# Performance work log

Hardware: AMD Instinct MI355X
Metric: run time of the kernel (lower is better)

The kernel has to match this reference:

```python
import jax, jax.numpy as jnp
import numpy as np
from jax import lax

B, T, N, C = 32, 32, 64, 64          # batch, window, num_series, inter_dim
GRU_H, QK, HOR = 64, 32, 12          # gru_dim, qk_dim, prediction_horizon
KS = (3, 5, 7)                       # temporal kernel per block (3 + 2*i)


def setup_inputs() -> dict:
    key = jax.random.key(0)
    ks = jax.random.split(key, 32)
    rn = lambda k, shape, s=0.05: jax.random.normal(k, shape, jnp.float32) * s
    inp = {"x": jax.random.normal(ks[0], (B, T, N), jnp.float32)}
    # x_to_inter_dim: Conv1d(1, C, kernel_size=1) == scalar * w + b
    inp["w_x2i"] = rn(ks[1], (C,)); inp["b_x2i"] = rn(ks[2], (C,))
    # latentCorrelation GRU (input_size=1, hidden=GRU_H), gate order r,z,n
    inp["gru_wih"] = rn(ks[3], (3 * GRU_H, 1)); inp["gru_whh"] = rn(ks[4], (3 * GRU_H, GRU_H))
    inp["gru_bih"] = rn(ks[5], (3 * GRU_H,)); inp["gru_bhh"] = rn(ks[6], (3 * GRU_H,))
    inp["wq_w"] = rn(ks[7], (QK, GRU_H)); inp["wq_b"] = rn(ks[8], (QK,))
    inp["wk_w"] = rn(ks[9], (QK, GRU_H)); inp["wk_b"] = rn(ks[10], (QK,))
    # per block: T independent GCNConvs (theta + bias), one temporal Conv1d
    for i, k_ in enumerate(KS):
        inp[f"gcn_w{i}"] = rn(ks[11 + 4 * i], (T, C, C))
        inp[f"gcn_b{i}"] = rn(ks[12 + 4 * i], (T, C))
        inp[f"conv_w{i}"] = rn(ks[13 + 4 * i], (C, C, k_))
        inp[f"conv_b{i}"] = rn(ks[14 + 4 * i], (C,))
    inp["lout_w"] = rn(ks[25], (N * HOR, T * N * C), 0.01)
    inp["lout_b"] = rn(ks[26], (N * HOR,))
    return inp


def _forward(x, w_x2i, b_x2i, gru_wih, gru_whh, gru_bih, gru_bhh,
             wq_w, wq_b, wk_w, wk_b,
             gcn_w0, gcn_b0, conv_w0, conv_b0,
             gcn_w1, gcn_b1, conv_w1, conv_b1,
             gcn_w2, gcn_b2, conv_w2, conv_b2,
             lout_w, lout_b):
    xs = jnp.transpose(x, (1, 0, 2))  # (T, B, N) time-major

    # --- latentCorrelation: one GRU run over all B*N series at once ---
    def gru_step(h, xt):  # h: (B,N,GRU_H), xt: (B,N)
        gi = xt[..., None] * gru_wih[:, 0] + gru_bih           # (B,N,3H)
        gh = h @ gru_whh.T + gru_bhh                           # (B,N,3H)
        r = jax.nn.sigmoid(gi[..., :GRU_H] + gh[..., :GRU_H])
        z = jax.nn.sigmoid(gi[..., GRU_H:2 * GRU_H] + gh[..., GRU_H:2 * GRU_H])
        n = jnp.tanh(gi[..., 2 * GRU_H:] + r * gh[..., 2 * GRU_H:])
        return (1.0 - z) * n + z * h, None

    h0 = jnp.zeros((B, N, GRU_H), x.dtype)
    hT, _ = lax.scan(gru_step, h0, xs)                         # (B,N,GRU_H)
    Q = hT @ wq_w.T + wq_b                                     # (B,N,QK)
    K = hT @ wk_w.T + wk_b
    Wadj = jax.nn.softmax(jnp.einsum('bnq,bmq->bnm', Q, K) / jnp.sqrt(jnp.float32(QK)), axis=2)

    # GCN symmetric norm on the dense complete graph; edge (src=i, tgt=j) has
    # weight Wadj[b,i,j]; degree is per-target (column) sum.
    deg = Wadj.sum(axis=1)                                     # (B,N)
    dinv = jnp.where(deg > 0, 1.0 / jnp.sqrt(deg), 0.0)
    What = dinv[:, :, None] * Wadj * dinv[:, None, :]          # (B,N,N)

    # x_to_inter_dim (1x1 conv) applied per timestep
    feats = xs[..., None] * w_x2i + b_x2i                      # (T,B,N,C)

    for gw, gb, cw, cb, k_ in ((gcn_w0, gcn_b0, conv_w0, conv_b0, 3),
                               (gcn_w1, gcn_b1, conv_w1, conv_b1, 5),
                               (gcn_w2, gcn_b2, conv_w2, conv_b2, 7)):
        xw = jnp.einsum('tbnc,tcd->tbnd', feats, gw)           # per-timestep theta
        agg = jnp.einsum('bij,tbid->tbjd', What, xw) + gb[:, None, None, :]
        seq = jnp.transpose(agg, (1, 2, 3, 0)).reshape(B * N, C, T)
        p = k_ // 2
        conv = lax.conv_general_dilated(seq, cw, (1,), [(p, p)],
                                        dimension_numbers=('NCH', 'OIH', 'NCH'))
        conv = conv + cb[None, :, None]
        conv = jnp.where(conv >= 0, conv, 0.01 * conv)         # LeakyReLU (dropout p=0)
        feats = jnp.transpose(conv.reshape(B, N, C, T), (3, 0, 1, 2))

    # stack(x_list, dim=2).view(B*N, C*T).view(B, -1) -> (B, N*C*T) feature order (n,c,t)
    flat = jnp.transpose(feats, (1, 2, 3, 0)).reshape(B, N * C * T)
    out = flat @ lout_w.T + lout_b                             # (B, N*HOR)
    return out.reshape(B, HOR, N)


def reference(x, w_x2i, b_x2i, gru_wih, gru_whh, gru_bih, gru_bhh,
              wq_w, wq_b, wk_w, wk_b,
              gcn_w0, gcn_b0, conv_w0, conv_b0,
              gcn_w1, gcn_b1, conv_w1, conv_b1,
              gcn_w2, gcn_b2, conv_w2, conv_b2,
              lout_w, lout_b):
    return _forward(x, w_x2i, b_x2i, gru_wih, gru_whh, gru_bih, gru_bhh,
                    wq_w, wq_b, wk_w, wk_b,
                    gcn_w0, gcn_b0, conv_w0, conv_b0,
                    gcn_w1, gcn_b1, conv_w1, conv_b1,
                    gcn_w2, gcn_b2, conv_w2, conv_b2,
                    lout_w, lout_b)
```

## Files before the change

### kernel.cpp

```cpp
#include <hip/hip_runtime.h>
#include <hip/hip_bf16.h>

#define BB 32
#define TT 32
#define NN 64
#define CC 64
#define HH 64
#define QKD 32
#define HOR 12
#define OUTD (NN*HOR)
#define KFLAT (NN*CC*TT)

typedef __attribute__((ext_vector_type(4))) float f32x4;
typedef __attribute__((ext_vector_type(8))) short s16x8;

static __device__ __forceinline__ unsigned short f2bf(float f) {
    unsigned u = __float_as_uint(f);
    unsigned r = (u + 0x7FFFu + ((u >> 16) & 1u)) >> 16;
    return (unsigned short)r;
}
static __device__ __forceinline__ float bf2f(unsigned short h) {
    return __uint_as_float(((unsigned)h) << 16);
}
static __device__ __forceinline__ void split8(const float* f, uint4& hi, uint4& lo) {
    unsigned hh[8], ll[8];
    #pragma unroll
    for (int i = 0; i < 8; ++i) {
        unsigned short h = f2bf(f[i]);
        float hf = bf2f(h);
        hh[i] = h;
        ll[i] = f2bf(f[i] - hf);
    }
    hi = make_uint4(hh[0] | (hh[1] << 16), hh[2] | (hh[3] << 16),
                    hh[4] | (hh[5] << 16), hh[6] | (hh[7] << 16));
    lo = make_uint4(ll[0] | (ll[1] << 16), ll[2] | (ll[3] << 16),
                    ll[4] | (ll[5] << 16), ll[6] | (ll[7] << 16));
}

__global__ __launch_bounds__(256) void gru_kernel(
    const float* __restrict__ x, const float* __restrict__ wih,
    const float* __restrict__ whh, const float* __restrict__ bih,
    const float* __restrict__ bhh, float* __restrict__ hT)
{
    __shared__ float Wt[64][192];
    __shared__ float hbuf[4][64];
    __shared__ float part[4][4][3][64];
    int tid = threadIdx.x;
    for (int idx = tid; idx < 192*64; idx += 256) {
        int g = idx >> 6, k = idx & 63;
        Wt[k][g] = whh[idx];
    }
    int w = tid >> 6;
    int j = tid & 63;
    hbuf[w][j] = 0.0f;
    __syncthreads();
    float Wreg[3][16];
    #pragma unroll
    for (int g = 0; g < 3; ++g)
        #pragma unroll
        for (int kk = 0; kk < 16; ++kk)
            Wreg[g][kk] = Wt[w*16 + kk][g*64 + j];
    int gs0 = blockIdx.x * 4;
    int b = gs0 >> 6, n0 = gs0 & 63;
    float wih_r = wih[j], wih_z = wih[64+j], wih_n = wih[128+j];
    float bi_r = bih[j], bi_z = bih[64+j], bi_n = bih[128+j];
    float bh_r = bhh[j], bh_z = bhh[64+j], bh_n = bhh[128+j];
    float hreg = 0.0f;
    for (int t = 0; t < TT; ++t) {
        float p[3][4];
        #pragma unroll
        for (int g = 0; g < 3; ++g)
            #pragma unroll
            for (int s = 0; s < 4; ++s) p[g][s] = 0.f;
        #pragma unroll
        for (int s = 0; s < 4; ++s) {
            #pragma unroll
            for (int q = 0; q < 4; ++q) {
                const float4 hv = *(const float4*)&hbuf[s][w*16 + q*4];
                #pragma unroll
                for (int g = 0; g < 3; ++g) {
                    p[g][s] += hv.x*Wreg[g][q*4]   + hv.y*Wreg[g][q*4+1]
                             + hv.z*Wreg[g][q*4+2] + hv.w*Wreg[g][q*4+3];
                }
            }
        }
        #pragma unroll
        for (int g = 0; g < 3; ++g)
            #pragma unroll
            for (int s = 0; s < 4; ++s)
                part[w][s][g][j] = p[g][s];
        __syncthreads();
        float gr = bh_r + part[0][w][0][j] + part[1][w][0][j] + part[2][w][0][j] + part[3][w][0][j];
        float gz = bh_z + part[0][w][1][j] + part[1][w][1][j] + part[2][w][1][j] + part[3][w][1][j];
        float gn = bh_n + part[0][w][2][j] + part[1][w][2][j] + part[2][w][2][j] + part[3][w][2][j];
        float xt = x[(b*TT + t)*NN + n0 + w];
        float r = 1.f/(1.f+__expf(-(xt*wih_r + bi_r + gr)));
        float z = 1.f/(1.f+__expf(-(xt*wih_z + bi_z + gz)));
        float nn_ = tanhf(xt*wih_n + bi_n + r*gn);
        float hnew = (1.f - z)*nn_ + z*hreg;
        hreg = hnew;
        hbuf[w][j] = hnew;
        __syncthreads();
    }
    hT[(gs0 + w)*64 + j] = hreg;
}

__global__ __launch_bounds__(256) void attn_kernel(
    const float* __restrict__ hT, const float* __restrict__ wq_w,
    const float* __restrict__ wq_b, const float* __restrict__ wk_w,
    const float* __restrict__ wk_b,
    unsigned short* __restrict__ whT_hi, unsigned short* __restrict__ whT_lo)
{
    __shared__ float hs[64][64];
    __shared__ float Qs[64][32], Ks[64][32];
    __shared__ float S[64][64];
    __shared__ float dinv[64];
    int b = blockIdx.x, tid = threadIdx.x;
    for (int idx = tid; idx < 64*64; idx += 256) hs[idx>>6][idx&63] = hT[b*4096 + idx];
    __syncthreads();
    for (int idx = tid; idx < 64*32; idx += 256) {
        int n_ = idx >> 5, q = idx & 31;
        float accq = wq_b[q], acck = wk_b[q];
        #pragma unroll 8
        for (int h_ = 0; h_ < 64; ++h_) {
            float hv = hs[n_][h_];
            accq += hv * wq_w[q*64 + h_];
            acck += hv * wk_w[q*64 + h_];
        }
        Qs[n_][q] = accq; Ks[n_][q] = acck;
    }
    __syncthreads();
    const float scale = 0.17677669529663687f;
    for (int idx = tid; idx < 64*64; idx += 256) {
        int n_ = idx >> 6, m = idx & 63;
        float acc = 0.f;
        #pragma unroll 8
        for (int q = 0; q < 32; ++q) acc += Qs[n_][q]*Ks[m][q];
        S[n_][m] = acc * scale;
    }
    __syncthreads();
    if (tid < 64) {
        float mx = -1e30f;
        for (int m = 0; m < 64; ++m) mx = fmaxf(mx, S[tid][m]);
        float sum = 0.f;
        for (int m = 0; m < 64; ++m) { float e = __expf(S[tid][m]-mx); S[tid][m] = e; sum += e; }
        float inv = 1.f/sum;
        for (int m = 0; m < 64; ++m) S[tid][m] *= inv;
    }
    __syncthreads();
    if (tid < 64) {
        float d = 0.f;
        for (int n_ = 0; n_ < 64; ++n_) d += S[n_][tid];
        dinv[tid] = (d > 0.f) ? 1.0f/sqrtf(d) : 0.f;
    }
    __syncthreads();
    for (int idx = tid; idx < 64*64; idx += 256) {
        int jj = idx >> 6, ii = idx & 63;
        float val = dinv[ii]*S[ii][jj]*dinv[jj];
        unsigned short h = f2bf(val);
        whT_hi[b*4096 + idx] = h;
        whT_lo[b*4096 + idx] = f2bf(val - bf2f(h));
    }
}

__global__ __launch_bounds__(256) void prep_uv(const float* __restrict__ gw0,
    const float* __restrict__ wx, const float* __restrict__ bx,
    float* __restrict__ u, float* __restrict__ v)
{
    __shared__ float pu[4][64], pv[4][64];
    int t = blockIdx.x, tid = threadIdx.x, d = tid & 63, cq = tid >> 6;
    float su = 0.f, sv = 0.f;
    for (int c = cq*16; c < cq*16 + 16; ++c) {
        float gv = gw0[t*4096 + c*64 + d];
        su += wx[c]*gv; sv += bx[c]*gv;
    }
    pu[cq][d] = su; pv[cq][d] = sv;
    __syncthreads();
    if (tid < 64) {
        u[t*64 + tid] = pu[0][tid]+pu[1][tid]+pu[2][tid]+pu[3][tid];
        v[t*64 + tid] = pv[0][tid]+pv[1][tid]+pv[2][tid]+pv[3][tid];
    }
}

__global__ __launch_bounds__(256) void prep_gwT(const float* __restrict__ gw,
    unsigned short* __restrict__ hi, unsigned short* __restrict__ lo)
{
    int t = blockIdx.x, tid = threadIdx.x;
    for (int idx = tid; idx < 4096; idx += 256) {
        int d = idx >> 6, c = idx & 63;
        float val = gw[t*4096 + c*64 + d];
        unsigned short h = f2bf(val);
        hi[t*4096 + idx] = h;
        lo[t*4096 + idx] = f2bf(val - bf2f(h));
    }
}

__global__ __launch_bounds__(256) void prep_cw(const float* __restrict__ cw,
    unsigned short* __restrict__ hi, unsigned short* __restrict__ lo, int KW)
{
    int co = blockIdx.x, tid = threadIdx.x, K = KW*64;
    for (int idx = tid; idx < K; idx += 256) {
        int ka = idx >> 6, ci = idx & 63;
        float val = cw[(size_t)(co*64 + ci)*KW + ka];
        unsigned short h = f2bf(val);
        hi[(size_t)co*K + idx] = h;
        lo[(size_t)co*K + idx] = f2bf(val - bf2f(h));
    }
}

template<bool FIRST>
__global__ __launch_bounds__(256) void gcn_mfma(
    const float* __restrict__ fin,
    const unsigned short* __restrict__ gwT_hi, const unsigned short* __restrict__ gwT_lo,
    const float* __restrict__ u, const float* __restrict__ v,
    const unsigned short* __restrict__ whT_hi, const unsigned short* __restrict__ whT_lo,
    const float* __restrict__ gb, float* __restrict__ o)
{
    __shared__ __align__(16) unsigned short ft_hi[64][64], ft_lo[64][64];
    __shared__ __align__(16) unsigned short xsT_hi[64][64], xsT_lo[64][64];
    __shared__ float x_l[64];
    int tb = blockIdx.x, t = tb >> 5, b = tb & 31;
    int tid = threadIdx.x;
    int w = tid >> 6, l = tid & 63, lm = l & 15, ld = l >> 4;

    if (FIRST) {
        if (tid < 64) x_l[tid] = fin[(b*TT + t)*NN + tid];
        __syncthreads();
        int d = tid >> 2, nq = tid & 3;
        float ud = u[t*64 + d], vd = v[t*64 + d];
        float vals[16];
        #pragma unroll
        for (int i = 0; i < 16; ++i) vals[i] = x_l[nq*16 + i]*ud + vd;
        #pragma unroll
        for (int h = 0; h < 2; ++h) {
            uint4 hi, lo; split8(&vals[h*8], hi, lo);
            int un = (nq*2 + h) ^ (d & 7);
            *(uint4*)&xsT_hi[d][un*8] = hi;
            *(uint4*)&xsT_lo[d][un*8] = lo;
        }
        __syncthreads();
    } else {
        {
            int row = tid >> 2, c0 = (tid & 3) * 16;
            const float* src = fin + (size_t)tb*4096 + row*64 + c0;
            float f8a[8], f8b[8];
            *(float4*)f8a = *(const float4*)src;       *(float4*)(f8a+4) = *(const float4*)(src+4);
            *(float4*)f8b = *(const float4*)(src+8);   *(float4*)(f8b+4) = *(const float4*)(src+12);
            uint4 hi, lo;
            split8(f8a, hi, lo);
            int u0 = ((c0>>3)) ^ (row & 7);
            *(uint4*)&ft_hi[row][u0*8] = hi; *(uint4*)&ft_lo[row][u0*8] = lo;
            split8(f8b, hi, lo);
            int u1 = ((c0>>3)+1) ^ (row & 7);
            *(uint4*)&ft_hi[row][u1*8] = hi; *(uint4*)&ft_lo[row][u1*8] = lo;
        }
        __syncthreads();
        f32x4 acc[4];
        #pragma unroll
        for (int ct = 0; ct < 4; ++ct) acc[ct] = (f32x4){0.f,0.f,0.f,0.f};
        #pragma unroll
        for (int kc = 0; kc < 2; ++kc) {
            int nrow = w*16 + lm;
            int ux = (kc*4 + ld) ^ (nrow & 7);
            s16x8 xh = *(const s16x8*)&ft_hi[nrow][ux*8];
            s16x8 xl = *(const s16x8*)&ft_lo[nrow][ux*8];
            #pragma unroll
            for (int ct = 0; ct < 4; ++ct) {
                int drow = ct*16 + lm;
                s16x8 yh = *(const s16x8*)&gwT_hi[t*4096 + drow*64 + kc*32 + ld*8];
                s16x8 yl = *(const s16x8*)&gwT_lo[t*4096 + drow*64 + kc*32 + ld*8];
                acc[ct] = __builtin_amdgcn_mfma_f32_16x16x32_bf16(xh, yh, acc[ct], 0, 0, 0);
                acc[ct] = __builtin_amdgcn_mfma_f32_16x16x32_bf16(xh, yl, acc[ct], 0, 0, 0);
                acc[ct] = __builtin_amdgcn_mfma_f32_16x16x32_bf16(xl, yh, acc[ct], 0, 0, 0);
            }
        }
        #pragma unroll
        for (int ct = 0; ct < 4; ++ct) {
            int d = ct*16 + lm;
            int n0 = w*16 + ld*4;
            unsigned short hh[4], llo[4];
            #pragma unroll
            for (int r = 0; r < 4; ++r) {
                float val = acc[ct][r];
                unsigned short h = f2bf(val);
                hh[r] = h; llo[r] = f2bf(val - bf2f(h));
            }
            int un = (n0 >> 3) ^ (d & 7);
            int base = d*64 + un*8 + (n0 & 7);
            *(uint2*)&xsT_hi[0][0 + base] = make_uint2(hh[0]|(hh[1]<<16), hh[2]|(hh[3]<<16));
            *(uint2*)&xsT_lo[0][0 + base] = make_uint2(llo[0]|(llo[1]<<16), llo[2]|(llo[3]<<16));
        }
        __syncthreads();
    }

    f32x4 acc2[4];
    #pragma unroll
    for (int ct = 0; ct < 4; ++ct) acc2[ct] = (f32x4){0.f,0.f,0.f,0.f};
    #pragma unroll
    for (int kc = 0; kc < 2; ++kc) {
        int jrow = w*16 + lm;
        s16x8 wh = *(const s16x8*)&whT_hi[b*4096 + jrow*64 + kc*32 + ld*8];
        s16x8 wl = *(const s16x8*)&whT_lo[b*4096 + jrow*64 + kc*32 + ld*8];
        #pragma unroll
        for (int ct = 0; ct < 4; ++ct) {
            int drow = ct*16 + lm;
            int uy = (kc*4 + ld) ^ (drow & 7);
            s16x8 yh = *(const s16x8*)&xsT_hi[drow][uy*8];
            s16x8 yl = *(const s16x8*)&xsT_lo[drow][uy*8];
            acc2[ct] = __builtin_amdgcn_mfma_f32_16x16x32_bf16(wh, yh, acc2[ct], 0, 0, 0);
            acc2[ct] = __builtin_amdgcn_mfma_f32_16x16x32_bf16(wh, yl, acc2[ct], 0, 0, 0);
            acc2[ct] = __builtin_amdgcn_mfma_f32_16x16x32_bf16(wl, yh, acc2[ct], 0, 0, 0);
        }
    }
    float* oo = o + (size_t)tb*4096;
    #pragma unroll
    for (int ct = 0; ct < 4; ++ct) {
        int d = ct*16 + lm;
        float bias = gb[t*64 + d];
        #pragma unroll
        for (int r = 0; r < 4; ++r) {
            int jj = w*16 + ld*4 + r;
            oo[jj*64 + d] = acc2[ct][r] + bias;
        }
    }
}

template<int KW>
__global__ __launch_bounds__(256) void conv_mfma(float* __restrict__ g,
    const unsigned short* __restrict__ wch, const unsigned short* __restrict__ wcl,
    const float* __restrict__ cb)
{
    constexpr int P = KW/2, K = KW*64, K32 = KW*2;
    __shared__ __align__(16) unsigned short sh[32][64], sl[32][64];
    int bn = blockIdx.x, tid = threadIdx.x;
    {
        int t = tid >> 3, c0 = (tid & 7) * 8;
        const float* src = &g[((size_t)t*2048 + bn)*64 + c0];
        float f8[8];
        *(float4*)f8 = *(const float4*)src;
        *(float4*)(f8+4) = *(const float4*)(src+4);
        uint4 hi, lo; split8(f8, hi, lo);
        int uu = (tid & 7) ^ (t & 7);
        *(uint4*)&sh[t][uu*8] = hi;
        *(uint4*)&sl[t][uu*8] = lo;
    }
    __syncthreads();
    int w = tid >> 6, l = tid & 63, lm = l & 15, ld = l >> 4;
    int co = w*16 + lm;
    f32x4 acc0 = {0.f,0.f,0.f,0.f}, acc1 = {0.f,0.f,0.f,0.f};
    const s16x8 zf = {0,0,0,0,0,0,0,0};
    for (int kc = 0; kc < K32; ++kc) {
        int ka = kc >> 1;
        int ci = (kc & 1)*32 + ld*8;
        s16x8 yh = *(const s16x8*)&wch[(size_t)co*K + kc*32 + ld*8];
        s16x8 yl = *(const s16x8*)&wcl[(size_t)co*K + kc*32 + ld*8];
        #pragma unroll
        for (int Mt = 0; Mt < 2; ++Mt) {
            int ts = Mt*16 + lm + ka - P;
            bool ok = ((unsigned)ts) < 32u;
            int tc = ok ? ts : 0;
            int ua = (ci >> 3) ^ (tc & 7);
            s16x8 xh = *(const s16x8*)&sh[tc][ua*8];
            s16x8 xl = *(const s16x8*)&sl[tc][ua*8];
            if (!ok) { xh = zf; xl = zf; }
            f32x4& a = Mt ? acc1 : acc0;
            a = __builtin_amdgcn_mfma_f32_16x16x32_bf16(xh, yh, a, 0, 0, 0);
            a = __builtin_amdgcn_mfma_f32_16x16x32_bf16(xh, yl, a, 0, 0, 0);
            a = __builtin_amdgcn_mfma_f32_16x16x32_bf16(xl, yh, a, 0, 0, 0);
        }
    }
    float bias = cb[co];
    #pragma unroll
    for (int Mt = 0; Mt < 2; ++Mt) {
        const f32x4& a = Mt ? acc1 : acc0;
        #pragma unroll
        for (int r = 0; r < 4; ++r) {
            int t = Mt*16 + ld*4 + r;
            float val = a[r] + bias;
            val = (val >= 0.f) ? val : 0.01f*val;
            g[((size_t)t*2048 + bn)*64 + co] = val;
        }
    }
}

__global__ void transpose_kernel(const float* __restrict__ f, unsigned short* __restrict__ o)
{
    __shared__ float tl[32][65];
    int bn = blockIdx.x;
    int tid = threadIdx.x;
    for (int idx = tid; idx < 2048; idx += 256) {
        int t = idx >> 6, c = idx & 63;
        tl[t][c] = f[((size_t)t*2048 + bn)*64 + c];
    }
    __syncthreads();
    int b = bn >> 6, n = bn & 63;
    unsigned short* ob = o + (size_t)b*KFLAT + n*2048;
    for (int idx = tid; idx < 2048; idx += 256) {
        int c = idx >> 5, t = idx & 31;
        ob[c*32 + t] = f2bf(tl[t][c]);
    }
}

__global__ void out_init(const float* __restrict__ bias, float* __restrict__ out)
{
    int idx = blockIdx.x*256 + threadIdx.x;
    out[idx] = bias[idx % OUTD];
}

__global__ __launch_bounds__(256) void gemm_mfma(const unsigned short* __restrict__ flat,
                                                 const float* __restrict__ W,
                                                 float* __restrict__ out)
{
    __shared__ __align__(16) float Wl[2][64][64];
    __shared__ __align__(16) unsigned short Al[2][32][64];
    const int tid = threadIdx.x;
    const int w = tid >> 6, l = tid & 63;
    const int og = blockIdx.x >> 6;
    const int kc = blockIdx.x & 63;
    const int o_blk = og * 64;
    const int kbase = kc * 2048;

    const int sb = tid >> 3, su = tid & 7;
    const size_t a_src = (size_t)sb * KFLAT + (unsigned)((su ^ (sb & 7)) * 8);

    float4 tw0, tw1, tw2, tw3; uint4 ta;

#define ISSUE(s_) { \
    int kwin_ = kbase + (s_)*64; \
    { int g_ = 0*256 + tid; int o_ = g_ >> 4; int u_ = g_ & 15; \
      tw0 = *(const float4*)&W[(size_t)(o_blk + o_)*KFLAT + kwin_ + ((u_ ^ (o_ & 7))*4)]; } \
    { int g_ = 1*256 + tid; int o_ = g_ >> 4; int u_ = g_ & 15; \
      tw1 = *(const float4*)&W[(size_t)(o_blk + o_)*KFLAT + kwin_ + ((u_ ^ (o_ & 7))*4)]; } \
    { int g_ = 2*256 + tid; int o_ = g_ >> 4; int u_ = g_ & 15; \
      tw2 = *(const float4*)&W[(size_t)(o_blk + o_)*KFLAT + kwin_ + ((u_ ^ (o_ & 7))*4)]; } \
    { int g_ = 3*256 + tid; int o_ = g_ >> 4; int u_ = g_ & 15; \
      tw3 = *(const float4*)&W[(size_t)(o_blk + o_)*KFLAT + kwin_ + ((u_ ^ (o_ & 7))*4)]; } \
    ta = *(const uint4*)&flat[a_src + kwin_]; }

#define COMMIT(nb_) { \
    { int g_ = 0*256 + tid; *(float4*)&Wl[nb_][g_>>4][(g_&15)*4] = tw0; } \
    { int g_ = 1*256 + tid; *(float4*)&Wl[nb_][g_>>4][(g_&15)*4] = tw1; } \
    { int g_ = 2*256 + tid; *(float4*)&Wl[nb_][g_>>4][(g_&15)*4] = tw2; } \
    { int g_ = 3*256 + tid; *(float4*)&Wl[nb_][g_>>4][(g_&15)*4] = tw3; } \
    *(uint4*)&Al[nb_][sb][su*8] = ta; }

    f32x4 acc0 = {0.f,0.f,0.f,0.f}, acc1 = {0.f,0.f,0.f,0.f};

    ISSUE(0);
    COMMIT(0);
    ISSUE(1);
    __syncthreads();

    const int lmod = l & 15, ldiv = l >> 4, lx = l & 7;
    int cur = 0;
    for (int s = 0; s < 32; ++s) {
        #pragma unroll
        for (int ksub = 0; ksub < 2; ++ksub) {
            int ju = ksub*8 + ldiv*2;
            const float4 b0 = *(const float4*)&Wl[cur][w*16 + lmod][(ju ^ lx)*4];
            const float4 b1 = *(const float4*)&Wl[cur][w*16 + lmod][((ju+1) ^ lx)*4];
            float bf[8] = {b0.x,b0.y,b0.z,b0.w,b1.x,b1.y,b1.z,b1.w};
            s16x8 bhi, blo;
            #pragma unroll
            for (int i = 0; i < 8; ++i) {
                unsigned short h = f2bf(bf[i]);
                float hf = bf2f(h);
                bhi[i] = (short)h;
                blo[i] = (short)f2bf(bf[i] - hf);
            }
            int jua = ksub*4 + ldiv;
            const s16x8 a0 = *(const s16x8*)&Al[cur][lmod]      [(jua ^ lx)*8];
            const s16x8 a1 = *(const s16x8*)&Al[cur][16 + lmod] [(jua ^ lx)*8];
            acc0 = __builtin_amdgcn_mfma_f32_16x16x32_bf16(a0, bhi, acc0, 0, 0, 0);
            acc0 = __builtin_amdgcn_mfma_f32_16x16x32_bf16(a0, blo, acc0, 0, 0, 0);
            acc1 = __builtin_amdgcn_mfma_f32_16x16x32_bf16(a1, bhi, acc1, 0, 0, 0);
            acc1 = __builtin_amdgcn_mfma_f32_16x16x32_bf16(a1, blo, acc1, 0, 0, 0);
        }
        if (s < 31) {
            COMMIT(cur^1);
            if (s < 30) ISSUE(s+2);
        }
        __syncthreads();
        cur ^= 1;
    }
#undef ISSUE
#undef COMMIT

    const int o_out = o_blk + w*16 + lmod;
    #pragma unroll
    for (int r = 0; r < 4; ++r) {
        int b0_ = ldiv*4 + r;
        atomicAdd(&out[(size_t)b0_*OUTD + o_out], acc0[r]);
        atomicAdd(&out[(size_t)(16 + b0_)*OUTD + o_out], acc1[r]);
    }
}

extern "C" void kernel_launch(void* const* d_in, const int* in_sizes, int n_in,
                              void* d_out, int out_size, void* d_ws, size_t ws_size,
                              hipStream_t stream) {
    (void)in_sizes; (void)n_in; (void)out_size; (void)ws_size;
    const float* x        = (const float*)d_in[0];
    const float* w_x2i    = (const float*)d_in[1];
    const float* b_x2i    = (const float*)d_in[2];
    const float* gru_wih  = (const float*)d_in[3];
    const float* gru_whh  = (const float*)d_in[4];
    const float* gru_bih  = (const float*)d_in[5];
    const float* gru_bhh  = (const float*)d_in[6];
    const float* wq_w     = (const float*)d_in[7];
    const float* wq_b     = (const float*)d_in[8];
    const float* wk_w     = (const float*)d_in[9];
    const float* wk_b     = (const float*)d_in[10];
    const float* gcn_w[3]  = {(const float*)d_in[11], (const float*)d_in[15], (const float*)d_in[19]};
    const float* gcn_b[3]  = {(const float*)d_in[12], (const float*)d_in[16], (const float*)d_in[20]};
    const float* conv_w[3] = {(const float*)d_in[13], (const float*)d_in[17], (const float*)d_in[21]};
    const float* conv_b[3] = {(const float*)d_in[14], (const float*)d_in[18], (const float*)d_in[22]};
    const float* lout_w   = (const float*)d_in[23];
    const float* lout_b   = (const float*)d_in[24];
    float* out = (float*)d_out;
    float* ws  = (float*)d_ws;

    float* hT   = ws;
    float* u    = ws + 131072;
    float* v    = ws + 133120;
    float* bufA = ws + 135168;
    float* bufB = bufA + 4194304;
    unsigned short* usb = (unsigned short*)(ws + 8523776);
    unsigned short* whT_hi  = usb;
    unsigned short* whT_lo  = usb + 131072;
    unsigned short* gwT1_hi = usb + 262144;
    unsigned short* gwT1_lo = usb + 393216;
    unsigned short* gwT2_hi = usb + 524288;
    unsigned short* gwT2_lo = usb + 655360;
    unsigned short* cw1_hi  = usb + 786432;
    unsigned short* cw1_lo  = usb + 798720;
    unsigned short* cw2_hi  = usb + 811008;
    unsigned short* cw2_lo  = usb + 831488;
    unsigned short* cw3_hi  = usb + 851968;
    unsigned short* cw3_lo  = usb + 880640;

    prep_uv<<<dim3(32), dim3(256), 0, stream>>>(gcn_w[0], w_x2i, b_x2i, u, v);
    prep_gwT<<<dim3(32), dim3(256), 0, stream>>>(gcn_w[1], gwT1_hi, gwT1_lo);
    prep_gwT<<<dim3(32), dim3(256), 0, stream>>>(gcn_w[2], gwT2_hi, gwT2_lo);
    prep_cw<<<dim3(64), dim3(256), 0, stream>>>(conv_w[0], cw1_hi, cw1_lo, 3);
    prep_cw<<<dim3(64), dim3(256), 0, stream>>>(conv_w[1], cw2_hi, cw2_lo, 5);
    prep_cw<<<dim3(64), dim3(256), 0, stream>>>(conv_w[2], cw3_hi, cw3_lo, 7);

    gru_kernel<<<dim3(512), dim3(256), 0, stream>>>(x, gru_wih, gru_whh, gru_bih, gru_bhh, hT);
    attn_kernel<<<dim3(32), dim3(256), 0, stream>>>(hT, wq_w, wq_b, wk_w, wk_b, whT_hi, whT_lo);

    gcn_mfma<true><<<dim3(1024), dim3(256), 0, stream>>>(x, nullptr, nullptr, u, v,
                                                         whT_hi, whT_lo, gcn_b[0], bufA);
    conv_mfma<3><<<dim3(2048), dim3(256), 0, stream>>>(bufA, cw1_hi, cw1_lo, conv_b[0]);
    gcn_mfma<false><<<dim3(1024), dim3(256), 0, stream>>>(bufA, gwT1_hi, gwT1_lo, u, v,
                                                          whT_hi, whT_lo, gcn_b[1], bufB);
    conv_mfma<5><<<dim3(2048), dim3(256), 0, stream>>>(bufB, cw2_hi, cw2_lo, conv_b[1]);
    gcn_mfma<false><<<dim3(1024), dim3(256), 0, stream>>>(bufB, gwT2_hi, gwT2_lo, u, v,
                                                          whT_hi, whT_lo, gcn_b[2], bufA);
    conv_mfma<7><<<dim3(2048), dim3(256), 0, stream>>>(bufA, cw3_hi, cw3_lo, conv_b[2]);

    unsigned short* flat16 = (unsigned short*)bufB;
    transpose_kernel<<<dim3(2048), dim3(256), 0, stream>>>(bufA, flat16);
    out_init<<<dim3(96), dim3(256), 0, stream>>>(lout_b, out);
    gemm_mfma<<<dim3(768), dim3(256), 0, stream>>>(flat16, lout_w, out);
}
```

Baseline: 344.9 us.

## Fuse prep kernels, fold transpose into last conv, async LDS loads in GEMM

```diff
diff --git a/kernel.cpp b/kernel.cpp
--- a/kernel.cpp
+++ b/kernel.cpp
@@ -36,13 +36,18 @@
     lo = make_uint4(ll[0] | (ll[1] << 16), ll[2] | (ll[3] << 16),
                     ll[4] | (ll[5] << 16), ll[6] | (ll[7] << 16));
 }
+static __device__ __forceinline__ void gl2lds16(const void* gsrc, void* ldst) {
+    __builtin_amdgcn_global_load_lds(
+        (const __attribute__((address_space(1))) unsigned int*)gsrc,
+        (__attribute__((address_space(3))) unsigned int*)ldst, 16, 0, 0);
+}
 
 __global__ __launch_bounds__(256) void gru_kernel(
     const float* __restrict__ x, const float* __restrict__ wih,
     const float* __restrict__ whh, const float* __restrict__ bih,
     const float* __restrict__ bhh, float* __restrict__ hT)
 {
-    __shared__ float Wt[64][192];
+    __shared__ float Wt[64][193];
     __shared__ float hbuf[4][64];
     __shared__ float part[4][4][3][64];
     int tid = threadIdx.x;
@@ -112,8 +117,9 @@
     unsigned short* __restrict__ whT_hi, unsigned short* __restrict__ whT_lo)
 {
     __shared__ float hs[64][64];
-    __shared__ float Qs[64][32], Ks[64][32];
-    __shared__ float S[64][64];
+    __shared__ float Qs[64][33], Ks[64][33];
+    __shared__ float S[64][65];
+    __shared__ float pd[4][64];
     __shared__ float dinv[64];
     int b = blockIdx.x, tid = threadIdx.x;
     for (int idx = tid; idx < 64*64; idx += 256) hs[idx>>6][idx&63] = hT[b*4096 + idx];
@@ -139,18 +145,34 @@
         S[n_][m] = acc * scale;
     }
     __syncthreads();
+    {
+        int r = tid >> 2, q = tid & 3;
+        float mx = -1e30f;
+        #pragma unroll
+        for (int m = 0; m < 16; ++m) mx = fmaxf(mx, S[r][q*16+m]);
+        mx = fmaxf(mx, __shfl_xor(mx, 1));
+        mx = fmaxf(mx, __shfl_xor(mx, 2));
+        float sum = 0.f;
+        float e[16];
+        #pragma unroll
+        for (int m = 0; m < 16; ++m) { e[m] = __expf(S[r][q*16+m]-mx); sum += e[m]; }
+        sum += __shfl_xor(sum, 1);
+        sum += __shfl_xor(sum, 2);
+        float inv = 1.f/sum;
+        #pragma unroll
+        for (int m = 0; m < 16; ++m) S[r][q*16+m] = e[m]*inv;
+    }
+    __syncthreads();
+    {
+        int c = tid & 63, rq = tid >> 6;
+        float d = 0.f;
+        #pragma unroll
+        for (int i = 0; i < 16; ++i) d += S[rq*16 + i][c];
+        pd[rq][c] = d;
+    }
+    __syncthreads();
     if (tid < 64) {
-        float mx = -1e30f;
-        for (int m = 0; m < 64; ++m) mx = fmaxf(mx, S[tid][m]);
-        float sum = 0.f;
-        for (int m = 0; m < 64; ++m) { float e = __expf(S[tid][m]-mx); S[tid][m] = e; sum += e; }
-        float inv = 1.f/sum;
-        for (int m = 0; m < 64; ++m) S[tid][m] *= inv;
-    }
-    __syncthreads();
-    if (tid < 64) {
-        float d = 0.f;
-        for (int n_ = 0; n_ < 64; ++n_) d += S[n_][tid];
+        float d = pd[0][tid]+pd[1][tid]+pd[2][tid]+pd[3][tid];
         dinv[tid] = (d > 0.f) ? 1.0f/sqrtf(d) : 0.f;
     }
     __syncthreads();
@@ -163,48 +185,59 @@
     }
 }
 
-__global__ __launch_bounds__(256) void prep_uv(const float* __restrict__ gw0,
-    const float* __restrict__ wx, const float* __restrict__ bx,
-    float* __restrict__ u, float* __restrict__ v)
+__global__ __launch_bounds__(256) void prep_all(
+    const float* __restrict__ gw0, const float* __restrict__ wx, const float* __restrict__ bx,
+    float* __restrict__ u, float* __restrict__ v,
+    const float* __restrict__ gw1, unsigned short* __restrict__ g1h, unsigned short* __restrict__ g1l,
+    const float* __restrict__ gw2, unsigned short* __restrict__ g2h, unsigned short* __restrict__ g2l,
+    const float* __restrict__ cw1, unsigned short* __restrict__ c1h, unsigned short* __restrict__ c1l,
+    const float* __restrict__ cw2, unsigned short* __restrict__ c2h, unsigned short* __restrict__ c2l,
+    const float* __restrict__ cw3, unsigned short* __restrict__ c3h, unsigned short* __restrict__ c3l,
+    const float* __restrict__ lb, float* __restrict__ out)
 {
-    __shared__ float pu[4][64], pv[4][64];
-    int t = blockIdx.x, tid = threadIdx.x, d = tid & 63, cq = tid >> 6;
-    float su = 0.f, sv = 0.f;
-    for (int c = cq*16; c < cq*16 + 16; ++c) {
-        float gv = gw0[t*4096 + c*64 + d];
-        su += wx[c]*gv; sv += bx[c]*gv;
-    }
-    pu[cq][d] = su; pv[cq][d] = sv;
-    __syncthreads();
-    if (tid < 64) {
-        u[t*64 + tid] = pu[0][tid]+pu[1][tid]+pu[2][tid]+pu[3][tid];
-        v[t*64 + tid] = pv[0][tid]+pv[1][tid]+pv[2][tid]+pv[3][tid];
-    }
-}
-
-__global__ __launch_bounds__(256) void prep_gwT(const float* __restrict__ gw,
-    unsigned short* __restrict__ hi, unsigned short* __restrict__ lo)
-{
-    int t = blockIdx.x, tid = threadIdx.x;
-    for (int idx = tid; idx < 4096; idx += 256) {
-        int d = idx >> 6, c = idx & 63;
-        float val = gw[t*4096 + c*64 + d];
-        unsigned short h = f2bf(val);
-        hi[t*4096 + idx] = h;
-        lo[t*4096 + idx] = f2bf(val - bf2f(h));
-    }
-}
-
-__global__ __launch_bounds__(256) void prep_cw(const float* __restrict__ cw,
-    unsigned short* __restrict__ hi, unsigned short* __restrict__ lo, int KW)
-{
-    int co = blockIdx.x, tid = threadIdx.x, K = KW*64;
-    for (int idx = tid; idx < K; idx += 256) {
-        int ka = idx >> 6, ci = idx & 63;
-        float val = cw[(size_t)(co*64 + ci)*KW + ka];
-        unsigned short h = f2bf(val);
-        hi[(size_t)co*K + idx] = h;
-        lo[(size_t)co*K + idx] = f2bf(val - bf2f(h));
+    int bid = blockIdx.x, tid = threadIdx.x;
+    if (bid < 32) {
+        __shared__ float pu[4][64], pv[4][64];
+        int t = bid, d = tid & 63, cq = tid >> 6;
+        float su = 0.f, sv = 0.f;
+        for (int c = cq*16; c < cq*16 + 16; ++c) {
+            float gv = gw0[t*4096 + c*64 + d];
+            su += wx[c]*gv; sv += bx[c]*gv;
+        }
+        pu[cq][d] = su; pv[cq][d] = sv;
+        __syncthreads();
+        if (tid < 64) {
+            u[t*64 + tid] = pu[0][tid]+pu[1][tid]+pu[2][tid]+pu[3][tid];
+            v[t*64 + tid] = pv[0][tid]+pv[1][tid]+pv[2][tid]+pv[3][tid];
+        }
+    } else if (bid < 96) {
+        const float* gw = (bid < 64) ? gw1 : gw2;
+        unsigned short* hi = (bid < 64) ? g1h : g2h;
+        unsigned short* lo = (bid < 64) ? g1l : g2l;
+        int t = (bid < 64) ? bid - 32 : bid - 64;
+        for (int idx = tid; idx < 4096; idx += 256) {
+            int d = idx >> 6, c = idx & 63;
+            float val = gw[t*4096 + c*64 + d];
+            unsigned short h = f2bf(val);
+            hi[t*4096 + idx] = h;
+            lo[t*4096 + idx] = f2bf(val - bf2f(h));
+        }
+    } else if (bid < 288) {
+        const float* cw; unsigned short *hi, *lo; int KW, co;
+        if (bid < 160)      { cw = cw1; hi = c1h; lo = c1l; KW = 3; co = bid - 96; }
+        else if (bid < 224) { cw = cw2; hi = c2h; lo = c2l; KW = 5; co = bid - 160; }
+        else                { cw = cw3; hi = c3h; lo = c3l; KW = 7; co = bid - 224; }
+        int K = KW*64;
+        for (int idx = tid; idx < K; idx += 256) {
+            int ka = idx >> 6, ci = idx & 63;
+            float val = cw[(size_t)(co*64 + ci)*KW + ka];
+            unsigned short h = f2bf(val);
+            hi[(size_t)co*K + idx] = h;
+            lo[(size_t)co*K + idx] = f2bf(val - bf2f(h));
+        }
+    } else {
+        int idx = (bid - 288)*256 + tid;
+        out[idx] = lb[idx % OUTD];
     }
 }
 
@@ -325,10 +358,10 @@
     }
 }
 
-template<int KW>
+template<int KW, bool LAST>
 __global__ __launch_bounds__(256) void conv_mfma(float* __restrict__ g,
     const unsigned short* __restrict__ wch, const unsigned short* __restrict__ wcl,
-    const float* __restrict__ cb)
+    const float* __restrict__ cb, unsigned short* __restrict__ fo)
 {
     constexpr int P = KW/2, K = KW*64, K32 = KW*2;
     __shared__ __align__(16) unsigned short sh[32][64], sl[32][64];
@@ -370,41 +403,34 @@
         }
     }
     float bias = cb[co];
-    #pragma unroll
-    for (int Mt = 0; Mt < 2; ++Mt) {
-        const f32x4& a = Mt ? acc1 : acc0;
-        #pragma unroll
-        for (int r = 0; r < 4; ++r) {
-            int t = Mt*16 + ld*4 + r;
-            float val = a[r] + bias;
-            val = (val >= 0.f) ? val : 0.01f*val;
-            g[((size_t)t*2048 + bn)*64 + co] = val;
-        }
-    }
-}
-
-__global__ void transpose_kernel(const float* __restrict__ f, unsigned short* __restrict__ o)
-{
-    __shared__ float tl[32][65];
-    int bn = blockIdx.x;
-    int tid = threadIdx.x;
-    for (int idx = tid; idx < 2048; idx += 256) {
-        int t = idx >> 6, c = idx & 63;
-        tl[t][c] = f[((size_t)t*2048 + bn)*64 + c];
-    }
-    __syncthreads();
-    int b = bn >> 6, n = bn & 63;
-    unsigned short* ob = o + (size_t)b*KFLAT + n*2048;
-    for (int idx = tid; idx < 2048; idx += 256) {
-        int c = idx >> 5, t = idx & 31;
-        ob[c*32 + t] = f2bf(tl[t][c]);
-    }
-}
-
-__global__ void out_init(const float* __restrict__ bias, float* __restrict__ out)
-{
-    int idx = blockIdx.x*256 + threadIdx.x;
-    out[idx] = bias[idx % OUTD];
+    if (LAST) {
+        int b = bn >> 6, n = bn & 63;
+        unsigned short* ob = fo + (size_t)b*KFLAT + n*2048 + co*32;
+        #pragma unroll
+        for (int Mt = 0; Mt < 2; ++Mt) {
+            const f32x4& a = Mt ? acc1 : acc0;
+            unsigned short hv[4];
+            #pragma unroll
+            for (int r = 0; r < 4; ++r) {
+                float val = a[r] + bias;
+                val = (val >= 0.f) ? val : 0.01f*val;
+                hv[r] = f2bf(val);
+            }
+            *(uint2*)&ob[Mt*16 + ld*4] = make_uint2(hv[0]|(hv[1]<<16), hv[2]|(hv[3]<<16));
+        }
+    } else {
+        #pragma unroll
+        for (int Mt = 0; Mt < 2; ++Mt) {
+            const f32x4& a = Mt ? acc1 : acc0;
+            #pragma unroll
+            for (int r = 0; r < 4; ++r) {
+                int t = Mt*16 + ld*4 + r;
+                float val = a[r] + bias;
+                val = (val >= 0.f) ? val : 0.01f*val;
+                g[((size_t)t*2048 + bn)*64 + co] = val;
+            }
+        }
+    }
 }
 
 __global__ __launch_bounds__(256) void gemm_mfma(const unsigned short* __restrict__ flat,
@@ -420,40 +446,37 @@
     const int o_blk = og * 64;
     const int kbase = kc * 2048;
 
-    const int sb = tid >> 3, su = tid & 7;
-    const size_t a_src = (size_t)sb * KFLAT + (unsigned)((su ^ (sb & 7)) * 8);
-
-    float4 tw0, tw1, tw2, tw3; uint4 ta;
-
-#define ISSUE(s_) { \
+    const int wrow_l = l >> 4;
+    const int wu = l & 15;
+    size_t w_off[4];
+    #pragma unroll
+    for (int i = 0; i < 4; ++i) {
+        int row = w*16 + i*4 + wrow_l;
+        w_off[i] = (size_t)(o_blk + row) * KFLAT + (unsigned)((wu ^ (row & 7)) * 4);
+    }
+    const int arow = w*8 + (l >> 3);
+    const int au = l & 7;
+    const size_t a_off0 = (size_t)arow * KFLAT + (unsigned)((au ^ (arow & 7)) * 8);
+
+#define ISSUE_TILE(buf_, s_) { \
     int kwin_ = kbase + (s_)*64; \
-    { int g_ = 0*256 + tid; int o_ = g_ >> 4; int u_ = g_ & 15; \
-      tw0 = *(const float4*)&W[(size_t)(o_blk + o_)*KFLAT + kwin_ + ((u_ ^ (o_ & 7))*4)]; } \
-    { int g_ = 1*256 + tid; int o_ = g_ >> 4; int u_ = g_ & 15; \
-      tw1 = *(const float4*)&W[(size_t)(o_blk + o_)*KFLAT + kwin_ + ((u_ ^ (o_ & 7))*4)]; } \
-    { int g_ = 2*256 + tid; int o_ = g_ >> 4; int u_ = g_ & 15; \
-      tw2 = *(const float4*)&W[(size_t)(o_blk + o_)*KFLAT + kwin_ + ((u_ ^ (o_ & 7))*4)]; } \
-    { int g_ = 3*256 + tid; int o_ = g_ >> 4; int u_ = g_ & 15; \
-      tw3 = *(const float4*)&W[(size_t)(o_blk + o_)*KFLAT + kwin_ + ((u_ ^ (o_ & 7))*4)]; } \
-    ta = *(const uint4*)&flat[a_src + kwin_]; }
-
-#define COMMIT(nb_) { \
-    { int g_ = 0*256 + tid; *(float4*)&Wl[nb_][g_>>4][(g_&15)*4] = tw0; } \
-    { int g_ = 1*256 + tid; *(float4*)&Wl[nb_][g_>>4][(g_&15)*4] = tw1; } \
-    { int g_ = 2*256 + tid; *(float4*)&Wl[nb_][g_>>4][(g_&15)*4] = tw2; } \
-    { int g_ = 3*256 + tid; *(float4*)&Wl[nb_][g_>>4][(g_&15)*4] = tw3; } \
-    *(uint4*)&Al[nb_][sb][su*8] = ta; }
+    _Pragma("unroll") \
+    for (int i_ = 0; i_ < 4; ++i_) \
+        gl2lds16(W + w_off[i_] + kwin_, &Wl[buf_][w*16 + i_*4][0]); \
+    gl2lds16(flat + a_off0 + kwin_, &Al[buf_][w*8][0]); \
+}
 
     f32x4 acc0 = {0.f,0.f,0.f,0.f}, acc1 = {0.f,0.f,0.f,0.f};
-
-    ISSUE(0);
-    COMMIT(0);
-    ISSUE(1);
-    __syncthreads();
+    ISSUE_TILE(0, 0);
+    ISSUE_TILE(1, 1);
 
     const int lmod = l & 15, ldiv = l >> 4, lx = l & 7;
-    int cur = 0;
     for (int s = 0; s < 32; ++s) {
+        if (s < 31) { asm volatile("s_waitcnt vmcnt(5)" ::: "memory"); }
+        else        { asm volatile("s_waitcnt vmcnt(0)" ::: "memory"); }
+        __builtin_amdgcn_s_barrier();
+        asm volatile("" ::: "memory");
+        const int cur = s & 1;
         #pragma unroll
         for (int ksub = 0; ksub < 2; ++ksub) {
             int ju = ksub*8 + ldiv*2;
@@ -476,15 +499,11 @@
             acc1 = __builtin_amdgcn_mfma_f32_16x16x32_bf16(a1, bhi, acc1, 0, 0, 0);
             acc1 = __builtin_amdgcn_mfma_f32_16x16x32_bf16(a1, blo, acc1, 0, 0, 0);
         }
-        if (s < 31) {
-            COMMIT(cur^1);
-            if (s < 30) ISSUE(s+2);
-        }
-        __syncthreads();
-        cur ^= 1;
-    }
-#undef ISSUE
-#undef COMMIT
+        asm volatile("" ::: "memory");
+        __builtin_amdgcn_s_barrier();
+        if (s < 30) { ISSUE_TILE(cur, s+2); }
+    }
+#undef ISSUE_TILE
 
     const int o_out = o_blk + w*16 + lmod;
     #pragma unroll
@@ -538,28 +557,28 @@
     unsigned short* cw3_hi  = usb + 851968;
     unsigned short* cw3_lo  = usb + 880640;
 
-    prep_uv<<<dim3(32), dim3(256), 0, stream>>>(gcn_w[0], w_x2i, b_x2i, u, v);
-    prep_gwT<<<dim3(32), dim3(256), 0, stream>>>(gcn_w[1], gwT1_hi, gwT1_lo);
-    prep_gwT<<<dim3(32), dim3(256), 0, stream>>>(gcn_w[2], gwT2_hi, gwT2_lo);
-    prep_cw<<<dim3(64), dim3(256), 0, stream>>>(conv_w[0], cw1_hi, cw1_lo, 3);
-    prep_cw<<<dim3(64), dim3(256), 0, stream>>>(conv_w[1], cw2_hi, cw2_lo, 5);
-    prep_cw<<<dim3(64), dim3(256), 0, stream>>>(conv_w[2], cw3_hi, cw3_lo, 7);
+    prep_all<<<dim3(384), dim3(256), 0, stream>>>(
+        gcn_w[0], w_x2i, b_x2i, u, v,
+        gcn_w[1], gwT1_hi, gwT1_lo,
+        gcn_w[2], gwT2_hi, gwT2_lo,
+        conv_w[0], cw1_hi, cw1_lo,
+        conv_w[1], cw2_hi, cw2_lo,
+        conv_w[2], cw3_hi, cw3_lo,
+        lout_b, out);
 
     gru_kernel<<<dim3(512), dim3(256), 0, stream>>>(x, gru_wih, gru_whh, gru_bih, gru_bhh, hT);
     attn_kernel<<<dim3(32), dim3(256), 0, stream>>>(hT, wq_w, wq_b, wk_w, wk_b, whT_hi, whT_lo);
 
+    unsigned short* flat16 = (unsigned short*)bufB;
     gcn_mfma<true><<<dim3(1024), dim3(256), 0, stream>>>(x, nullptr, nullptr, u, v,
                                                          whT_hi, whT_lo, gcn_b[0], bufA);
-    conv_mfma<3><<<dim3(2048), dim3(256), 0, stream>>>(bufA, cw1_hi, cw1_lo, conv_b[0]);
+    conv_mfma<3,false><<<dim3(2048), dim3(256), 0, stream>>>(bufA, cw1_hi, cw1_lo, conv_b[0], nullptr);
     gcn_mfma<false><<<dim3(1024), dim3(256), 0, stream>>>(bufA, gwT1_hi, gwT1_lo, u, v,
                                                           whT_hi, whT_lo, gcn_b[1], bufB);
-    conv_mfma<5><<<dim3(2048), dim3(256), 0, stream>>>(bufB, cw2_hi, cw2_lo, conv_b[1]);
+    conv_mfma<5,false><<<dim3(2048), dim3(256), 0, stream>>>(bufB, cw2_hi, cw2_lo, conv_b[1], nullptr);
     gcn_mfma<false><<<dim3(1024), dim3(256), 0, stream>>>(bufB, gwT2_hi, gwT2_lo, u, v,
                                                           whT_hi, whT_lo, gcn_b[2], bufA);
-    conv_mfma<7><<<dim3(2048), dim3(256), 0, stream>>>(bufA, cw3_hi, cw3_lo, conv_b[2]);
-
-    unsigned short* flat16 = (unsigned short*)bufB;
-    transpose_kernel<<<dim3(2048), dim3(256), 0, stream>>>(bufA, flat16);
-    out_init<<<dim3(96), dim3(256), 0, stream>>>(lout_b, out);
+    conv_mfma<7,true><<<dim3(2048), dim3(256), 0, stream>>>(bufA, cw3_hi, cw3_lo, conv_b[2], (unsigned short*)bufB);
+
     gemm_mfma<<<dim3(768), dim3(256), 0, stream>>>(flat16, lout_w, out);
 }
```

Measured after the change: 307.8 us. -10.8%, faster.
